# Performance work log

Measured on AMD Instinct MI355X. Metric: run time of the kernel, lower is better.

The kernel has to match this reference:

```python
import jax, jax.numpy as jnp
import numpy as np

B, ID, OD = 4096, 2048, 1024


def _conv_softmax(x, w):
    # x: [..., L]; torch Conv1d(1,1,k=3,stride=1,pad=1,bias=False) then softmax(dim=-1)
    L = x.shape[-1]
    xp = jnp.pad(x, [(0, 0)] * (x.ndim - 1) + [(1, 1)])
    y = w[0] * xp[..., 0:L] + w[1] * xp[..., 1:L + 1] + w[2] * xp[..., 2:L + 2]
    return jax.nn.softmax(y, axis=-1)


def _lstm_cell(x, h, c, Wih, Whh, bih, bhh):
    # torch LSTMCell gate order: i, f, g, o
    g = x @ Wih.T + h @ Whh.T + (bih + bhh)
    i, f, gg, o = jnp.split(g, 4, axis=-1)
    c2 = jax.nn.sigmoid(f) * c + jax.nn.sigmoid(i) * jnp.tanh(gg)
    h2 = jax.nn.sigmoid(o) * jnp.tanh(c2)
    return h2, c2


def _lstm_params(key, in_dim, hid):
    k = 1.0 / np.sqrt(hid)
    ks = jax.random.split(key, 4)
    Wih = jax.random.uniform(ks[0], (4 * hid, in_dim), jnp.float32, -k, k)
    Whh = jax.random.uniform(ks[1], (4 * hid, hid), jnp.float32, -k, k)
    bih = jax.random.uniform(ks[2], (4 * hid,), jnp.float32, -k, k)
    bhh = jax.random.uniform(ks[3], (4 * hid,), jnp.float32, -k, k)
    return Wih, Whh, bih, bhh


def setup_inputs() -> dict:
    key = jax.random.key(0)
    ks = jax.random.split(key, 12)
    spec = jax.random.normal(ks[0], (B, ID), jnp.float32)
    Wih1, Whh1, bih1, bhh1 = _lstm_params(ks[1], ID, OD)
    Wih2, Whh2, bih2, bhh2 = _lstm_params(ks[2], ID // 2, OD // 2)
    Wih3, Whh3, bih3, bhh3 = _lstm_params(ks[3], ID // 4, OD // 4)
    Wih4, Whh4, bih4, bhh4 = _lstm_params(ks[4], ID // 8, OD // 8)
    ck = np.sqrt(1.0 / 3.0)  # Conv1d(1,1,3) init bound
    w2_1h = jax.random.uniform(ks[5], (3,), jnp.float32, -ck, ck)
    w2_1c = jax.random.uniform(ks[6], (3,), jnp.float32, -ck, ck)
    w3_2h = jax.random.uniform(ks[7], (3,), jnp.float32, -ck, ck)
    w3_2c = jax.random.uniform(ks[8], (3,), jnp.float32, -ck, ck)
    w4_3h = jax.random.uniform(ks[9], (3,), jnp.float32, -ck, ck)
    w4_3c = jax.random.uniform(ks[10], (3,), jnp.float32, -ck, ck)
    return dict(spec=spec,
                Wih1=Wih1, Whh1=Whh1, bih1=bih1, bhh1=bhh1,
                Wih2=Wih2, Whh2=Whh2, bih2=bih2, bhh2=bhh2,
                Wih3=Wih3, Whh3=Whh3, bih3=bih3, bhh3=bhh3,
                Wih4=Wih4, Whh4=Whh4, bih4=bih4, bhh4=bhh4,
                w2_1h=w2_1h, w2_1c=w2_1c, w3_2h=w3_2h, w3_2c=w3_2c,
                w4_3h=w4_3h, w4_3c=w4_3c)


def reference(spec, Wih1, Whh1, bih1, bhh1, Wih2, Whh2, bih2, bhh2,
              Wih3, Whh3, bih3, bhh3, Wih4, Whh4, bih4, bhh4,
              w2_1h, w2_1c, w3_2h, w3_2c, w4_3h, w4_3c):
    b = spec.shape[0]
    # Level 4: 8 independent steps, fresh zero state each (torch code passes no hidden)
    x4 = spec.reshape(b, 8, ID // 8)
    z4 = jnp.zeros((b, 8, OD // 8), spec.dtype)
    h4, c4 = _lstm_cell(x4, z4, z4, Wih4, Whh4, bih4, bhh4)   # [b,8,OD/8]
    hb4 = _conv_softmax(h4.reshape(b, 4, OD // 4), w4_3h)      # pairs -> [b,4,OD/4]
    cb4 = _conv_softmax(c4.reshape(b, 4, OD // 4), w4_3c)
    # Level 3: 4 independent steps seeded by level-4 blended states
    x3 = spec.reshape(b, 4, ID // 4)
    h3, c3 = _lstm_cell(x3, hb4, cb4, Wih3, Whh3, bih3, bhh3)  # [b,4,OD/4]
    hb3 = _conv_softmax(h3.reshape(b, 2, OD // 2), w3_2h)      # [b,2,OD/2]
    cb3 = _conv_softmax(c3.reshape(b, 2, OD // 2), w3_2c)
    # Level 2: 2 independent steps
    x2 = spec.reshape(b, 2, ID // 2)
    h2, c2 = _lstm_cell(x2, hb3, cb3, Wih2, Whh2, bih2, bhh2)  # [b,2,OD/2]
    hb2 = _conv_softmax(h2.reshape(b, OD), w2_1h)              # [b,OD]
    cb2 = _conv_softmax(c2.reshape(b, OD), w2_1c)
    # Level 1: single full-resolution step; forward returns out1 = h1
    h1, c1 = _lstm_cell(spec, hb2, cb2, Wih1, Whh1, bih1, bhh1)
    return h1
```

## Files before the change

kernel.cpp:

```cpp
#include <hip/hip_runtime.h>


typedef __bf16 bf16x8 __attribute__((ext_vector_type(8)));
typedef float f32x4 __attribute__((ext_vector_type(4)));
typedef unsigned short u16x4 __attribute__((ext_vector_type(4)));

#define AS1 __attribute__((address_space(1)))
#define AS3 __attribute__((address_space(3)))

__device__ __forceinline__ unsigned short f2bf(float f) {
    union { float f; unsigned int i; } v; v.f = f;
    unsigned int r = v.i + 0x7fffu + ((v.i >> 16) & 1u);
    return (unsigned short)(r >> 16);
}
__device__ __forceinline__ float sigm(float x) { return 1.f / (1.f + __expf(-x)); }
__device__ __forceinline__ float tanh_(float x) { float e = __expf(2.f * x); return 1.f - 2.f / (e + 1.f); }

__global__ __launch_bounds__(256) void cvt_spec3(
    const float* __restrict__ spec, unsigned short* __restrict__ sB,
    unsigned short* __restrict__ X, unsigned short* __restrict__ Y, long n4)
{
    const long stride = (long)gridDim.x * blockDim.x;
    for (long i = (long)blockIdx.x * blockDim.x + threadIdx.x; i < n4; i += stride) {
        const float4 v = ((const float4*)spec)[i];
        u16x4 o; o.x = f2bf(v.x); o.y = f2bf(v.y); o.z = f2bf(v.z); o.w = f2bf(v.w);
        ((u16x4*)sB)[i] = o;
        const long b = i >> 9;
        const int c4 = (int)(i & 511);
        *(u16x4*)(X + (b * 4 + (c4 >> 7)) * 768  + ((c4 & 127) << 2)) = o;
        *(u16x4*)(Y + (b * 2 + (c4 >> 8)) * 1536 + ((c4 & 255) << 2)) = o;
    }
}

__global__ __launch_bounds__(256) void cvt_specA(
    const float* __restrict__ spec, unsigned short* __restrict__ dst, long n4)
{
    const long stride = (long)gridDim.x * blockDim.x;
    for (long i = (long)blockIdx.x * blockDim.x + threadIdx.x; i < n4; i += stride) {
        const float4 v = ((const float4*)spec)[i];
        const long m = i >> 9;
        const int col = ((int)(i & 511)) << 2;
        u16x4 o; o.x = f2bf(v.x); o.y = f2bf(v.y); o.z = f2bf(v.z); o.w = f2bf(v.w);
        *(u16x4*)(dst + m * 3072 + col) = o;
    }
}

struct PSeg { const float* src; unsigned short* dst; long g0; int H; int kshift; int dstld; int dstcol; };
struct PArgs { PSeg s[7]; long total; };

__global__ __launch_bounds__(256) void cvt_permW_all(PArgs pa)
{
    const long stride = (long)gridDim.x * blockDim.x;
    for (long gi = (long)blockIdx.x * blockDim.x + threadIdx.x; gi < pa.total; gi += stride) {
        int si = 0;
#pragma unroll
        for (int k = 1; k < 7; ++k) si += (gi >= pa.s[k].g0);
        const PSeg sg = pa.s[si];
        const long i = gi - sg.g0;
        const int kq = 1 << sg.kshift;
        const int p = (int)(i >> sg.kshift);
        const int kk = ((int)i & (kq - 1)) << 2;
        const int o = ((p >> 6) << 4) | (p & 15);
        const int q = (p >> 4) & 3;
        const long r = (long)q * sg.H + o;
        const float4 v = *(const float4*)(sg.src + (r << (sg.kshift + 2)) + kk);
        u16x4 wv; wv.x = f2bf(v.x); wv.y = f2bf(v.y); wv.z = f2bf(v.z); wv.w = f2bf(v.w);
        *(u16x4*)(sg.dst + (long)p * sg.dstld + sg.dstcol + kk) = wv;
    }
}

__global__ __launch_bounds__(256) void bias_all(
    const float* __restrict__ bih1, const float* __restrict__ bhh1,
    const float* __restrict__ bih2, const float* __restrict__ bhh2,
    const float* __restrict__ bih3, const float* __restrict__ bhh3,
    const float* __restrict__ bih4, const float* __restrict__ bhh4,
    float* __restrict__ bs1, float* __restrict__ bs2,
    float* __restrict__ bs3, float* __restrict__ bs4)
{
    const int i = blockIdx.x * 256 + threadIdx.x;
    const float *bih, *bhh; float* dst; int H, j;
    if (i < 4096)      { bih = bih1; bhh = bhh1; dst = bs1; H = 1024; j = i; }
    else if (i < 6144) { bih = bih2; bhh = bhh2; dst = bs2; H = 512;  j = i - 4096; }
    else if (i < 7168) { bih = bih3; bhh = bhh3; dst = bs3; H = 256;  j = i - 6144; }
    else               { bih = bih4; bhh = bhh4; dst = bs4; H = 128;  j = i - 7168; }
    const int o = ((j >> 6) << 4) | (j & 15);
    const int q = (j >> 4) & 3;
    dst[j] = bih[q * H + o] + bhh[q * H + o];
}

#define QUAD(AF, S, NS, BF)                                                                 \
    { _Pragma("unroll") for (int mi = 0; mi < 4; ++mi) {                                    \
        _Pragma("unroll") for (int ni = 0; ni < 2; ++ni) {                                  \
            acc[(S)*4+mi][(NS)*2+ni] = __builtin_amdgcn_mfma_f32_16x16x32_bf16(             \
                AF[mi][0], BF[ni][0], acc[(S)*4+mi][(NS)*2+ni], 0, 0, 0);                   \
            acc[(S)*4+mi][(NS)*2+ni] = __builtin_amdgcn_mfma_f32_16x16x32_bf16(             \
                AF[mi][1], BF[ni][1], acc[(S)*4+mi][(NS)*2+ni], 0, 0, 0);                   \
    } } }

#define GLL(gsrc, loff) __builtin_amdgcn_global_load_lds(                                   \
    (const AS1 void*)(gsrc), (AS3 void*)(lds + (loff)), 16, 0, 0)

#define FENCE asm volatile("" ::: "memory")

template<bool HAS_CIN, bool LAST>
__global__ __launch_bounds__(512, 2) void gemm8(
    const unsigned short* __restrict__ A, const unsigned short* __restrict__ W, const int K,
    const float* __restrict__ bsum, const float* __restrict__ Cin,
    float* __restrict__ Hout, float* __restrict__ Cout, const int H)
{
    __shared__ __align__(16) char lds[131072];
    const int t = threadIdx.x;
    const int w = t >> 6, l = t & 63;
    const int wr = w >> 2, wc = w & 3;

    const int GX = gridDim.x, GY = gridDim.y;
    const int nwg = GX * GY;
    const int bid = (int)blockIdx.y * GX + (int)blockIdx.x;
    const int swz = (bid & 7) * (nwg >> 3) + (bid >> 3);
    const int m0 = (swz / GY) * 256, n0 = (swz % GY) * 256;

    const int colsw = ((l & 7) ^ (l >> 3)) * 8;
    const size_t k128 = (size_t)128 * K;
    const size_t aoff0 = (size_t)(m0 + w * 16 + (l >> 3)) * K + colsw;
    const size_t aoff1 = aoff0 + (size_t)8 * K;
    const size_t boff0 = (size_t)(n0 + w * 16 + (l >> 3)) * K + colsw;
    const size_t boff1 = boff0 + (size_t)8 * K;
    const int sd0 = w * 2048 + l * 16;
    const int sd1 = sd0 + 1024;

    const int lr128 = (l & 15) * 128;
    const int sw0 = (((l >> 4)    ) ^ (l & 7)) * 16;
    const int sw1 = (((l >> 4) + 4) ^ (l & 7)) * 16;

    f32x4 acc[8][4];
#pragma unroll
    for (int i = 0; i < 8; ++i)
#pragma unroll
        for (int j = 0; j < 4; ++j) acc[i][j] = (f32x4){0.f, 0.f, 0.f, 0.f};

    const int NT = K >> 6;

    GLL(A + aoff0, sd0);                      GLL(A + aoff1, sd1);
    GLL(A + aoff0 + k128, 16384 + sd0);       GLL(A + aoff1 + k128, 16384 + sd1);
    GLL(W + boff0, 32768 + sd0);              GLL(W + boff1, 32768 + sd1);
    GLL(W + boff0 + k128, 49152 + sd0);       GLL(W + boff1 + k128, 49152 + sd1);
    GLL(W + boff0 + 64, 98304 + sd0);         GLL(W + boff1 + 64, 98304 + sd1);
    GLL(W + boff0 + k128 + 64, 114688 + sd0); GLL(W + boff1 + k128 + 64, 114688 + sd1);

    bf16x8 aLo[4][2], aHi[4][2], bF0[2][2], bF1[2][2];

    for (int tt = 0; tt < NT; ++tt) {
        const int q = tt & 1, qn = q ^ 1;
        const int rbA = (q << 16) + (wr << 14) + lr128;
        const int rbB = (q << 16) + 32768 + wc * 8192 + lr128;
        const bool st1 = (tt + 1 < NT), st2 = (tt + 2 < NT);

        if (st1) { asm volatile("s_waitcnt vmcnt(4)" ::: "memory"); }
        else     { asm volatile("s_waitcnt vmcnt(0)" ::: "memory"); }
        __builtin_amdgcn_s_barrier();
        FENCE;

#pragma unroll
        for (int mi = 0; mi < 4; ++mi) {
            aLo[mi][0] = *(const bf16x8*)(lds + rbA + mi * 2048 + sw0);
            aLo[mi][1] = *(const bf16x8*)(lds + rbA + mi * 2048 + sw1);
        }
#pragma unroll
        for (int ni = 0; ni < 2; ++ni) {
            bF0[ni][0] = *(const bf16x8*)(lds + rbB + ni * 2048 + sw0);
            bF0[ni][1] = *(const bf16x8*)(lds + rbB + ni * 2048 + sw1);
            bF1[ni][0] = *(const bf16x8*)(lds + rbB + 4096 + ni * 2048 + sw0);
            bF1[ni][1] = *(const bf16x8*)(lds + rbB + 4096 + ni * 2048 + sw1);
        }
        if (st1) {
            const size_t ko1 = (size_t)(tt + 1) * 64;
            GLL(A + aoff0 + ko1, (qn << 16) + sd0);
            GLL(A + aoff1 + ko1, (qn << 16) + sd1);
            GLL(A + aoff0 + k128 + ko1, (qn << 16) + 16384 + sd0);
            GLL(A + aoff1 + k128 + ko1, (qn << 16) + 16384 + sd1);
        }
#pragma unroll
        for (int mi = 0; mi < 4; ++mi) {
            aHi[mi][0] = *(const bf16x8*)(lds + rbA + 8192 + mi * 2048 + sw0);
            aHi[mi][1] = *(const bf16x8*)(lds + rbA + 8192 + mi * 2048 + sw1);
        }

        __builtin_amdgcn_s_setprio(1);
        QUAD(aLo, 0, 0, bF0);
        QUAD(aLo, 0, 1, bF1);
        __builtin_amdgcn_s_setprio(0);
        __builtin_amdgcn_s_barrier();
        FENCE;

        if (st2) {
            const size_t ko2 = (size_t)(tt + 2) * 64;
            GLL(W + boff0 + ko2, (q << 16) + 32768 + sd0);
            GLL(W + boff1 + ko2, (q << 16) + 32768 + sd1);
            GLL(W + boff0 + k128 + ko2, (q << 16) + 49152 + sd0);
            GLL(W + boff1 + k128 + ko2, (q << 16) + 49152 + sd1);
        }
        __builtin_amdgcn_s_setprio(1);
        QUAD(aHi, 1, 1, bF1);
        QUAD(aHi, 1, 0, bF0);
        __builtin_amdgcn_s_setprio(0);
    }

    const int ocol = (n0 >> 6) * 16 + wc * 16 + (l & 15);
    const int bb = n0 + wc * 64 + (l & 15);
    const float b0 = bsum[bb], b1 = bsum[bb + 16], b2 = bsum[bb + 32], b3 = bsum[bb + 48];
    const int mrow0 = m0 + wr * 128 + (l >> 4) * 4;
#pragma unroll
    for (int mi = 0; mi < 8; ++mi)
#pragma unroll
        for (int j = 0; j < 4; ++j) {
            const size_t m = (size_t)(mrow0 + mi * 16 + j);
            const float gi = acc[mi][0][j] + b0;
            const float gf = acc[mi][1][j] + b1;
            const float gg = acc[mi][2][j] + b2;
            const float go = acc[mi][3][j] + b3;
            float c2 = sigm(gi) * tanh_(gg);
            if (HAS_CIN) c2 += sigm(gf) * Cin[m * H + ocol];
            const float h2 = sigm(go) * tanh_(c2);
            Hout[m * H + ocol] = h2;
            if (!LAST) Cout[m * H + ocol] = c2;
        }
}

template<int L>
__global__ __launch_bounds__(256) void conv_dual(
    const float* __restrict__ Hin, const float* __restrict__ Cin,
    const float* __restrict__ w3h, const float* __restrict__ w3c,
    unsigned short* __restrict__ Yb, int ldYb, float* __restrict__ cbuf)
{
    __shared__ float xs[L + 2];
    __shared__ float red[8];
    const int nrows = gridDim.x >> 1;
    const bool isC = (int)blockIdx.x >= nrows;
    const int row = isC ? ((int)blockIdx.x - nrows) : (int)blockIdx.x;
    const float* Xs = isC ? Cin : Hin;
    const float* w3 = isC ? w3c : w3h;
    const int t = threadIdx.x;
    const size_t base = (size_t)row * L;
    const float w0 = w3[0], w1 = w3[1], w2 = w3[2];
    if (t == 0) { xs[0] = 0.f; xs[L + 1] = 0.f; }
    for (int i = t; i < L; i += 256) xs[i + 1] = Xs[base + i];
    __syncthreads();
    constexpr int E = L / 256;
    float y[E];
    float vmax = -3.4e38f;
#pragma unroll
    for (int i = 0; i < E; ++i) {
        const int c = t + i * 256;
        y[i] = w0 * xs[c] + w1 * xs[c + 1] + w2 * xs[c + 2];
        vmax = fmaxf(vmax, y[i]);
    }
#pragma unroll
    for (int off = 32; off >= 1; off >>= 1) vmax = fmaxf(vmax, __shfl_xor(vmax, off));
    if ((t & 63) == 0) red[t >> 6] = vmax;
    __syncthreads();
    vmax = fmaxf(fmaxf(red[0], red[1]), fmaxf(red[2], red[3]));
    float s = 0.f;
#pragma unroll
    for (int i = 0; i < E; ++i) { y[i] = __expf(y[i] - vmax); s += y[i]; }
#pragma unroll
    for (int off = 32; off >= 1; off >>= 1) s += __shfl_xor(s, off);
    if ((t & 63) == 0) red[4 + (t >> 6)] = s;
    __syncthreads();
    const float inv = 1.f / (red[4] + red[5] + red[6] + red[7]);
#pragma unroll
    for (int i = 0; i < E; ++i) {
        const int c = t + i * 256;
        const float v = y[i] * inv;
        if (isC) cbuf[base + c] = v;
        else     Yb[(size_t)row * ldYb + c] = f2bf(v);
    }
}

extern "C" void kernel_launch(void* const* d_in, const int* in_sizes, int n_in,
                              void* d_out, int out_size, void* d_ws, size_t ws_size,
                              hipStream_t stream)
{
    (void)in_sizes; (void)n_in; (void)out_size; (void)ws_size;
    const float* spec  = (const float*)d_in[0];
    const float* Wih1  = (const float*)d_in[1];
    const float* Whh1  = (const float*)d_in[2];
    const float* bih1  = (const float*)d_in[3];
    const float* bhh1  = (const float*)d_in[4];
    const float* Wih2  = (const float*)d_in[5];
    const float* Whh2  = (const float*)d_in[6];
    const float* bih2  = (const float*)d_in[7];
    const float* bhh2  = (const float*)d_in[8];
    const float* Wih3  = (const float*)d_in[9];
    const float* Whh3  = (const float*)d_in[10];
    const float* bih3  = (const float*)d_in[11];
    const float* bhh3  = (const float*)d_in[12];
    const float* Wih4  = (const float*)d_in[13];
    const float* bih4  = (const float*)d_in[15];
    const float* bhh4  = (const float*)d_in[16];
    const float* w2_1h = (const float*)d_in[17];
    const float* w2_1c = (const float*)d_in[18];
    const float* w3_2h = (const float*)d_in[19];
    const float* w3_2c = (const float*)d_in[20];
    const float* w4_3h = (const float*)d_in[21];
    const float* w4_3c = (const float*)d_in[22];

    char* ws = (char*)d_ws;
    float*          h   = (float*)(ws + 0);
    float*          c   = (float*)(ws + (size_t)16777216);
    float*          cb  = (float*)(ws + (size_t)33554432);
    unsigned short* sB  = (unsigned short*)(ws + (size_t)50331648);
    unsigned short* X   = (unsigned short*)(ws + (size_t)67108864);
    unsigned short* Y   = (unsigned short*)(ws + (size_t)92274688);
    unsigned short* Wc1 = (unsigned short*)(ws + (size_t)117440512);
    unsigned short* Wc2 = (unsigned short*)(ws + (size_t)142606336);
    unsigned short* Wc3 = (unsigned short*)(ws + (size_t)148897792);
    unsigned short* W4  = (unsigned short*)(ws + (size_t)150470656);
    float*          bs1 = (float*)(ws + (size_t)150732800);
    float*          bs2 = bs1 + 4096;
    float*          bs3 = bs2 + 4096;
    float*          bs4 = bs3 + 4096;

    cvt_spec3<<<2048, 256, 0, stream>>>(spec, sB, X, Y, 2097152);
    PArgs pa;
    pa.s[0] = { Wih1, Wc1,       0, 1024, 9, 3072,    0 };
    pa.s[1] = { Whh1, Wc1, 2097152, 1024, 8, 3072, 2048 };
    pa.s[2] = { Wih2, Wc2, 3145728,  512, 8, 1536,    0 };
    pa.s[3] = { Whh2, Wc2, 3670016,  512, 7, 1536, 1024 };
    pa.s[4] = { Wih3, Wc3, 3932160,  256, 7,  768,    0 };
    pa.s[5] = { Whh3, Wc3, 4063232,  256, 6,  768,  512 };
    pa.s[6] = { Wih4, W4,  4128768,  128, 6,  256,    0 };
    pa.total = 4161536;
    cvt_permW_all<<<2048, 256, 0, stream>>>(pa);
    bias_all<<<30, 256, 0, stream>>>(bih1, bhh1, bih2, bhh2, bih3, bhh3, bih4, bhh4,
                                     bs1, bs2, bs3, bs4);

    gemm8<false, false><<<dim3(128, 2), 512, 0, stream>>>(sB, W4, 256, bs4, nullptr, h, c, 128);
    conv_dual<256><<<32768, 256, 0, stream>>>(h, c, w4_3h, w4_3c, X + 512, 768, cb);

    gemm8<true, false><<<dim3(64, 4), 512, 0, stream>>>(X, Wc3, 768, bs3, cb, h, c, 256);
    cvt_specA<<<2048, 256, 0, stream>>>(spec, X, 2097152);
    conv_dual<512><<<16384, 256, 0, stream>>>(h, c, w3_2h, w3_2c, Y + 1024, 1536, cb);

    gemm8<true, false><<<dim3(32, 8), 512, 0, stream>>>(Y, Wc2, 1536, bs2, cb, h, c, 512);
    conv_dual<1024><<<8192, 256, 0, stream>>>(h, c, w2_1h, w2_1c, X + 2048, 3072, cb);

    gemm8<true, true><<<dim3(16, 16), 512, 0, stream>>>(X, Wc1, 3072, bs1, cb, (float*)d_out, nullptr, 1024);
}
```

Before: 309.9 us.

## Restructure GEMM main loop into four interleaved phases with fragment prefetch

Rewrites the bf16 MFMA main loop in the LSTM gate GEMM so each K-tile runs in four phases. Each phase overlaps a subset of LDS fragment reads and async global-to-LDS loads with one quadrant of MFMAs, separated by barriers. The next tile's aLo/bF0 fragments are loaded before the last quadrant so LDS latency hides behind compute. The cost is more barriers per iteration and more register pressure, and the reordered waits and LDS buffer reuse risk races if they do not line up.

```diff
diff --git a/kernel.cpp b/kernel.cpp
--- a/kernel.cpp
+++ b/kernel.cpp
@@ -100,8 +100,6 @@
 #define GLL(gsrc, loff) __builtin_amdgcn_global_load_lds(                                   \
     (const AS1 void*)(gsrc), (AS3 void*)(lds + (loff)), 16, 0, 0)
 
-#define FENCE asm volatile("" ::: "memory")
-
 template<bool HAS_CIN, bool LAST>
 __global__ __launch_bounds__(512, 2) void gemm8(
     const unsigned short* __restrict__ A, const unsigned short* __restrict__ W, const int K,
@@ -146,62 +144,94 @@
     GLL(W + boff0 + k128, 49152 + sd0);       GLL(W + boff1 + k128, 49152 + sd1);
     GLL(W + boff0 + 64, 98304 + sd0);         GLL(W + boff1 + 64, 98304 + sd1);
     GLL(W + boff0 + k128 + 64, 114688 + sd0); GLL(W + boff1 + k128 + 64, 114688 + sd1);
+    asm volatile("s_waitcnt vmcnt(4)" ::: "memory");
+    __builtin_amdgcn_s_barrier();
 
     bf16x8 aLo[4][2], aHi[4][2], bF0[2][2], bF1[2][2];
+
+    {
+        const int rbA = (wr << 14) + lr128;
+        const int rbB = 32768 + wc * 8192 + lr128;
+#pragma unroll
+        for (int mi = 0; mi < 4; ++mi) {
+            aLo[mi][0] = *(const bf16x8*)(lds + rbA + mi * 2048 + sw0);
+            aLo[mi][1] = *(const bf16x8*)(lds + rbA + mi * 2048 + sw1);
+        }
+#pragma unroll
+        for (int ni = 0; ni < 2; ++ni) {
+            bF0[ni][0] = *(const bf16x8*)(lds + rbB + ni * 2048 + sw0);
+            bF0[ni][1] = *(const bf16x8*)(lds + rbB + ni * 2048 + sw1);
+        }
+    }
 
     for (int tt = 0; tt < NT; ++tt) {
         const int q = tt & 1, qn = q ^ 1;
-        const int rbA = (q << 16) + (wr << 14) + lr128;
-        const int rbB = (q << 16) + 32768 + wc * 8192 + lr128;
+        const int rbA  = (q << 16) + (wr << 14) + lr128;
+        const int rbB  = (q << 16) + 32768 + wc * 8192 + lr128;
+        const int rbA2 = (qn << 16) + (wr << 14) + lr128;
+        const int rbB2 = (qn << 16) + 32768 + wc * 8192 + lr128;
         const bool st1 = (tt + 1 < NT), st2 = (tt + 2 < NT);
-
+        const size_t ko1 = (size_t)(tt + 1) * 64;
+        const size_t ko2 = (size_t)(tt + 2) * 64;
+
+#pragma unroll
+        for (int mi = 0; mi < 4; ++mi) {
+            aHi[mi][0] = *(const bf16x8*)(lds + rbA + 8192 + mi * 2048 + sw0);
+            aHi[mi][1] = *(const bf16x8*)(lds + rbA + 8192 + mi * 2048 + sw1);
+        }
+        if (st1) {
+            GLL(A + aoff0 + ko1, (qn << 16) + sd0);
+            GLL(A + aoff1 + ko1, (qn << 16) + sd1);
+        }
+        __builtin_amdgcn_s_barrier();
+        __builtin_amdgcn_s_setprio(1);
+        QUAD(aLo, 0, 0, bF0);
+        __builtin_amdgcn_s_setprio(0);
+
+#pragma unroll
+        for (int ni = 0; ni < 2; ++ni) {
+            bF1[ni][0] = *(const bf16x8*)(lds + rbB + 4096 + ni * 2048 + sw0);
+            bF1[ni][1] = *(const bf16x8*)(lds + rbB + 4096 + ni * 2048 + sw1);
+        }
+        if (st1) {
+            GLL(A + aoff0 + k128 + ko1, (qn << 16) + 16384 + sd0);
+            GLL(A + aoff1 + k128 + ko1, (qn << 16) + 16384 + sd1);
+        }
+        __builtin_amdgcn_s_barrier();
+        __builtin_amdgcn_s_setprio(1);
+        QUAD(aHi, 1, 0, bF0);
+        __builtin_amdgcn_s_setprio(0);
+
+        if (st2) {
+            GLL(W + boff0 + ko2, (q << 16) + 32768 + sd0);
+            GLL(W + boff1 + ko2, (q << 16) + 32768 + sd1);
+        }
+        __builtin_amdgcn_s_barrier();
+        __builtin_amdgcn_s_setprio(1);
+        QUAD(aLo, 0, 1, bF1);
+        __builtin_amdgcn_s_setprio(0);
+
+        if (st2) {
+            GLL(W + boff0 + k128 + ko2, (q << 16) + 49152 + sd0);
+            GLL(W + boff1 + k128 + ko2, (q << 16) + 49152 + sd1);
+        }
         if (st1) { asm volatile("s_waitcnt vmcnt(4)" ::: "memory"); }
         else     { asm volatile("s_waitcnt vmcnt(0)" ::: "memory"); }
         __builtin_amdgcn_s_barrier();
-        FENCE;
-
-#pragma unroll
-        for (int mi = 0; mi < 4; ++mi) {
-            aLo[mi][0] = *(const bf16x8*)(lds + rbA + mi * 2048 + sw0);
-            aLo[mi][1] = *(const bf16x8*)(lds + rbA + mi * 2048 + sw1);
-        }
-#pragma unroll
-        for (int ni = 0; ni < 2; ++ni) {
-            bF0[ni][0] = *(const bf16x8*)(lds + rbB + ni * 2048 + sw0);
-            bF0[ni][1] = *(const bf16x8*)(lds + rbB + ni * 2048 + sw1);
-            bF1[ni][0] = *(const bf16x8*)(lds + rbB + 4096 + ni * 2048 + sw0);
-            bF1[ni][1] = *(const bf16x8*)(lds + rbB + 4096 + ni * 2048 + sw1);
-        }
         if (st1) {
-            const size_t ko1 = (size_t)(tt + 1) * 64;
-            GLL(A + aoff0 + ko1, (qn << 16) + sd0);
-            GLL(A + aoff1 + ko1, (qn << 16) + sd1);
-            GLL(A + aoff0 + k128 + ko1, (qn << 16) + 16384 + sd0);
-            GLL(A + aoff1 + k128 + ko1, (qn << 16) + 16384 + sd1);
-        }
-#pragma unroll
-        for (int mi = 0; mi < 4; ++mi) {
-            aHi[mi][0] = *(const bf16x8*)(lds + rbA + 8192 + mi * 2048 + sw0);
-            aHi[mi][1] = *(const bf16x8*)(lds + rbA + 8192 + mi * 2048 + sw1);
-        }
-
-        __builtin_amdgcn_s_setprio(1);
-        QUAD(aLo, 0, 0, bF0);
-        QUAD(aLo, 0, 1, bF1);
-        __builtin_amdgcn_s_setprio(0);
-        __builtin_amdgcn_s_barrier();
-        FENCE;
-
-        if (st2) {
-            const size_t ko2 = (size_t)(tt + 2) * 64;
-            GLL(W + boff0 + ko2, (q << 16) + 32768 + sd0);
-            GLL(W + boff1 + ko2, (q << 16) + 32768 + sd1);
-            GLL(W + boff0 + k128 + ko2, (q << 16) + 49152 + sd0);
-            GLL(W + boff1 + k128 + ko2, (q << 16) + 49152 + sd1);
+#pragma unroll
+            for (int mi = 0; mi < 4; ++mi) {
+                aLo[mi][0] = *(const bf16x8*)(lds + rbA2 + mi * 2048 + sw0);
+                aLo[mi][1] = *(const bf16x8*)(lds + rbA2 + mi * 2048 + sw1);
+            }
+#pragma unroll
+            for (int ni = 0; ni < 2; ++ni) {
+                bF0[ni][0] = *(const bf16x8*)(lds + rbB2 + ni * 2048 + sw0);
+                bF0[ni][1] = *(const bf16x8*)(lds + rbB2 + ni * 2048 + sw1);
+            }
         }
         __builtin_amdgcn_s_setprio(1);
         QUAD(aHi, 1, 1, bF1);
-        QUAD(aHi, 1, 0, bF0);
         __builtin_amdgcn_s_setprio(0);
     }
 
```

After: 313.8 us. Within noise of the previous version (+1.3%).
